# Optimization experiments

Measured on AMD Instinct MI355X. Metric: run time of the kernel, lower is better.

Reference implementation:

```python
import jax, jax.numpy as jnp
import numpy as np

N = 65536   # number of feature vectors (feat_num)
D = 512     # feature dim (feat_size)
NC = 256    # number of unique classes n; N % NC == 0 as required by feat.chunk(n, 0)
EPS = 1e-8  # torch nn.CosineSimilarity eps


def setup_inputs() -> dict:
    key = jax.random.key(0)
    feat = jax.random.normal(key, (N, D), dtype=jnp.float32)
    # contiguous class blocks so chunk(n,0) groups match unique labels (module's implicit assumption)
    label = (jnp.arange(N, dtype=jnp.int32) // (N // NC)).astype(jnp.int32)
    return {"feat": feat, "label": label}


def reference(feat, label):
    n = NC  # len(label.unique()); static by construction
    # per-class centers: mean of each contiguous chunk  -> [n, D]
    centers = feat.reshape(n, N // n, D).mean(axis=1)
    # pairwise cosine similarity (torch CosineSimilarity: dot / (max(|x|,eps)*max(|y|,eps)))
    norms = jnp.sqrt(jnp.sum(centers * centers, axis=1, keepdims=True))  # [n,1]
    normed = centers / jnp.maximum(norms, EPS)
    sim = normed @ normed.T  # [n, n]
    # mask = label1 eq label1^T; labels are unique -> identity mask. Off-diagonal min per row.
    eye = jnp.eye(n, dtype=bool)
    dist_an = jnp.min(jnp.where(eye, jnp.inf, sim), axis=1)  # [n]
    # sum_i (1 - min_j!=i sim[i,j])
    return jnp.sum(1.0 - dist_an)
```

## Files before the change

### kernel.cpp

```cpp
#include <hip/hip_runtime.h>
#include <math.h>

#define NFEAT 65536
#define DIM   512
#define D4    128
#define NCLS  256
#define ROWS_PER_CLASS 256
#define EPSV  1e-8f

typedef float vf4 __attribute__((ext_vector_type(4)));

__global__ __launch_bounds__(1024)
void kA_center_norm(const vf4* __restrict__ feat4, float4* __restrict__ nT4,
                    float* __restrict__ out) {
    const int cls  = blockIdx.x;
    const int t    = threadIdx.x;
    const int col4 = t & 127;
    const int sub  = t >> 7;
    const int row0 = cls * ROWS_PER_CLASS + sub * 32;

    const vf4* p = feat4 + (size_t)row0 * D4 + col4;

    vf4 v[8], w[8];
#pragma unroll
    for (int k = 0; k < 8; ++k)
        v[k] = __builtin_nontemporal_load(p + (size_t)k * D4);

    vf4 acc = (vf4){0.f, 0.f, 0.f, 0.f};
#pragma unroll
    for (int r = 8; r < 32; r += 8) {
#pragma unroll
        for (int k = 0; k < 8; ++k)
            w[k] = __builtin_nontemporal_load(p + (size_t)(r + k) * D4);
#pragma unroll
        for (int k = 0; k < 8; ++k) {
            acc += v[k];
            v[k] = w[k];
        }
    }
#pragma unroll
    for (int k = 0; k < 8; ++k) acc += v[k];

    __shared__ vf4 red[1024];
    red[t] = acc;
    __syncthreads();

    __shared__ float wsum[2];
    __shared__ float s_inv;
    vf4 c = (vf4){0.f, 0.f, 0.f, 0.f};
    if (t < 128) {
        c = red[t];
#pragma unroll
        for (int s = 1; s < 8; ++s) c += red[t + 128 * s];
        const float ms = 1.0f / (float)ROWS_PER_CLASS;
        c *= ms;

        float ss = c.x*c.x + c.y*c.y + c.z*c.z + c.w*c.w;
#pragma unroll
        for (int o = 32; o > 0; o >>= 1) ss += __shfl_down(ss, o, 64);
        if ((t & 63) == 0) wsum[t >> 6] = ss;
    }
    __syncthreads();
    if (t == 0) {
        float nrm = sqrtf(wsum[0] + wsum[1]);
        s_inv = 1.0f / fmaxf(nrm, EPSV);
        if (cls == 0) out[0] = 0.f;
    }
    __syncthreads();
    if (t < 128) {
        c *= s_inv;
        float4 o4 = make_float4(c.x, c.y, c.z, c.w);
        nT4[(size_t)col4 * NCLS + cls] = o4;
    }
}

__global__ __launch_bounds__(1024)
void kB_min_sum(const float4* __restrict__ nT4, float* __restrict__ out) {
    const int j = blockIdx.x;
    const int t = threadIdx.x;

    __shared__ float4 bj[D4];
    __shared__ float  pacc[4][256];
    __shared__ float  wmin[4];
    if (t < D4) bj[t] = nT4[(size_t)t * NCLS + j];
    __syncthreads();

    const int i    = t & 255;
    const int part = t >> 8;
    const int g0   = part * 32;
    float dacc = 0.f;
#pragma unroll 8
    for (int g = g0; g < g0 + 32; ++g) {
        float4 a = nT4[(size_t)g * NCLS + i];
        float4 b = bj[g];
        dacc += a.x*b.x + a.y*b.y + a.z*b.z + a.w*b.w;
    }
    pacc[part][i] = dacc;
    __syncthreads();

    if (t < 256) {
        float d = pacc[0][i] + pacc[1][i] + pacc[2][i] + pacc[3][i];
        if (i == j) d = INFINITY;
#pragma unroll
        for (int o = 32; o > 0; o >>= 1) d = fminf(d, __shfl_down(d, o, 64));
        if ((i & 63) == 0) wmin[i >> 6] = d;
    }
    __syncthreads();
    if (t == 0) {
        float m = fminf(fminf(wmin[0], wmin[1]), fminf(wmin[2], wmin[3]));
        atomicAdd(out, 1.0f - m);
    }
}

extern "C" void kernel_launch(void* const* d_in, const int* in_sizes, int n_in,
                              void* d_out, int out_size, void* d_ws, size_t ws_size,
                              hipStream_t stream) {
    const float* feat = (const float*)d_in[0];
    float* out = (float*)d_out;

    float* nT4f = (float*)d_ws;

    kA_center_norm <<<NCLS, 1024, 0, stream>>>((const vf4*)feat, (float4*)nT4f, out);
    kB_min_sum     <<<NCLS, 1024, 0, stream>>>((const float4*)nT4f, out);
}
```

Measured before the change: 188.2 us.

## Split center reduction into many small partial-sum blocks plus a normalize kernel

The class-center pass is split in two. The first kernel uses 2048 blocks of 128 threads, each summing 32 rows into a partial vector in workspace. A second small kernel combines the 8 partials per class, normalizes, and writes the transposed layout. This spreads the 128 MB streaming read over more, smaller blocks for better occupancy and memory-level parallelism than 256 large blocks, at the cost of an extra launch and a small partial-sum round trip.

```diff
diff --git a/kernel.cpp b/kernel.cpp
--- a/kernel.cpp
+++ b/kernel.cpp
@@ -10,16 +10,13 @@
 
 typedef float vf4 __attribute__((ext_vector_type(4)));
 
-__global__ __launch_bounds__(1024)
-void kA_center_norm(const vf4* __restrict__ feat4, float4* __restrict__ nT4,
-                    float* __restrict__ out) {
-    const int cls  = blockIdx.x;
-    const int t    = threadIdx.x;
-    const int col4 = t & 127;
-    const int sub  = t >> 7;
-    const int row0 = cls * ROWS_PER_CLASS + sub * 32;
+__global__ __launch_bounds__(128, 4)
+void kA1_partial(const vf4* __restrict__ feat4, vf4* __restrict__ part) {
+    const int g = blockIdx.x;
+    const int t = threadIdx.x;
+    const int row0 = (g >> 3) * ROWS_PER_CLASS + (g & 7) * 32;
 
-    const vf4* p = feat4 + (size_t)row0 * D4 + col4;
+    const vf4* p = feat4 + (size_t)row0 * D4 + t;
 
     vf4 v[8], w[8];
 #pragma unroll
@@ -41,37 +38,38 @@
 #pragma unroll
     for (int k = 0; k < 8; ++k) acc += v[k];
 
-    __shared__ vf4 red[1024];
-    red[t] = acc;
-    __syncthreads();
+    part[(size_t)g * 128 + t] = acc;
+}
+
+__global__ __launch_bounds__(128)
+void kA2_norm(const vf4* __restrict__ part, float4* __restrict__ nT4,
+              float* __restrict__ out) {
+    const int c = blockIdx.x;
+    const int t = threadIdx.x;
+
+    const vf4* q = part + (size_t)c * 8 * 128 + t;
+    vf4 cs = q[0];
+#pragma unroll
+    for (int s = 1; s < 8; ++s) cs += q[(size_t)s * 128];
+    const float ms = 1.0f / (float)ROWS_PER_CLASS;
+    cs *= ms;
+
+    float ss = cs.x*cs.x + cs.y*cs.y + cs.z*cs.z + cs.w*cs.w;
+#pragma unroll
+    for (int o = 32; o > 0; o >>= 1) ss += __shfl_down(ss, o, 64);
 
     __shared__ float wsum[2];
     __shared__ float s_inv;
-    vf4 c = (vf4){0.f, 0.f, 0.f, 0.f};
-    if (t < 128) {
-        c = red[t];
-#pragma unroll
-        for (int s = 1; s < 8; ++s) c += red[t + 128 * s];
-        const float ms = 1.0f / (float)ROWS_PER_CLASS;
-        c *= ms;
-
-        float ss = c.x*c.x + c.y*c.y + c.z*c.z + c.w*c.w;
-#pragma unroll
-        for (int o = 32; o > 0; o >>= 1) ss += __shfl_down(ss, o, 64);
-        if ((t & 63) == 0) wsum[t >> 6] = ss;
-    }
+    if ((t & 63) == 0) wsum[t >> 6] = ss;
     __syncthreads();
     if (t == 0) {
         float nrm = sqrtf(wsum[0] + wsum[1]);
         s_inv = 1.0f / fmaxf(nrm, EPSV);
-        if (cls == 0) out[0] = 0.f;
+        if (c == 0) out[0] = 0.f;
     }
     __syncthreads();
-    if (t < 128) {
-        c *= s_inv;
-        float4 o4 = make_float4(c.x, c.y, c.z, c.w);
-        nT4[(size_t)col4 * NCLS + cls] = o4;
-    }
+    cs *= s_inv;
+    nT4[(size_t)t * NCLS + c] = make_float4(cs.x, cs.y, cs.z, cs.w);
 }
 
 __global__ __launch_bounds__(1024)
@@ -85,9 +83,9 @@
     if (t < D4) bj[t] = nT4[(size_t)t * NCLS + j];
     __syncthreads();
 
-    const int i    = t & 255;
-    const int part = t >> 8;
-    const int g0   = part * 32;
+    const int i  = t & 255;
+    const int pt = t >> 8;
+    const int g0 = pt * 32;
     float dacc = 0.f;
 #pragma unroll 8
     for (int g = g0; g < g0 + 32; ++g) {
@@ -95,7 +93,7 @@
         float4 b = bj[g];
         dacc += a.x*b.x + a.y*b.y + a.z*b.z + a.w*b.w;
     }
-    pacc[part][i] = dacc;
+    pacc[pt][i] = dacc;
     __syncthreads();
 
     if (t < 256) {
@@ -119,7 +117,9 @@
     float* out = (float*)d_out;
 
     float* nT4f = (float*)d_ws;
+    vf4*   prt  = (vf4*)((char*)d_ws + 512 * 1024);
 
-    kA_center_norm <<<NCLS, 1024, 0, stream>>>((const vf4*)feat, (float4*)nT4f, out);
-    kB_min_sum     <<<NCLS, 1024, 0, stream>>>((const float4*)nT4f, out);
+    kA1_partial<<<2048, 128, 0, stream>>>((const vf4*)feat, prt);
+    kA2_norm   <<<NCLS,  128, 0, stream>>>(prt, (float4*)nT4f, out);
+    kB_min_sum <<<NCLS, 1024, 0, stream>>>((const float4*)nT4f, out);
 }
```

After: 191.7 us. About the same (+1.9%).

## Stream class rows through double-buffered LDS via global_load_lds in center kernel

Applied to the files above, without the earlier changes.

The per-class reduction kernel now copies feature rows straight from global memory into two 64KB LDS stage buffers with global_load_lds, double-buffering eight 64KB chunks. Each chunk is summed by one group of 128 threads while the next loads. The goal is to keep many loads in flight and skip register staging for this bandwidth-bound 128MB read. In exchange, 128KB of shared memory limits each CU to one block, only one eighth of the threads do adds per chunk, and two barriers per chunk serialize the loop.

```diff
diff --git a/kernel.cpp b/kernel.cpp
--- a/kernel.cpp
+++ b/kernel.cpp
@@ -1,5 +1,6 @@
 #include <hip/hip_runtime.h>
 #include <math.h>
+#include <stdint.h>
 
 #define NFEAT 65536
 #define DIM   512
@@ -10,52 +11,80 @@
 
 typedef float vf4 __attribute__((ext_vector_type(4)));
 
+#define SFENCE() __builtin_amdgcn_sched_barrier(0)
+#define AS1C(p) ((const __attribute__((address_space(1))) void*)(p))
+#define AS3(p)  ((__attribute__((address_space(3))) void*)(p))
+
 __global__ __launch_bounds__(1024)
-void kA_center_norm(const vf4* __restrict__ feat4, float4* __restrict__ nT4,
+void kA_center_norm(const float* __restrict__ feat, float4* __restrict__ nT4,
                     float* __restrict__ out) {
     const int cls  = blockIdx.x;
     const int t    = threadIdx.x;
+    const int w    = t >> 6;
+    const int lane = t & 63;
     const int col4 = t & 127;
     const int sub  = t >> 7;
-    const int row0 = cls * ROWS_PER_CLASS + sub * 32;
 
-    const vf4* p = feat4 + (size_t)row0 * D4 + col4;
+    __shared__ char stage[2][65536];
 
-    vf4 v[8], w[8];
-#pragma unroll
-    for (int k = 0; k < 8; ++k)
-        v[k] = __builtin_nontemporal_load(p + (size_t)k * D4);
+    const char* cbase = (const char*)feat + (size_t)cls * (ROWS_PER_CLASS * DIM * 4);
+    const char* gsrc  = cbase + (size_t)w * 1024 + (size_t)lane * 16;
+
+#define ISSUE(c, p) do {                                                      \
+        const char* g_ = gsrc + (size_t)(c) * 65536;                          \
+        char* l_ = &stage[p][w * 1024];                                       \
+        __builtin_amdgcn_global_load_lds(AS1C(g_),         AS3(l_),         16, 0, 0); \
+        __builtin_amdgcn_global_load_lds(AS1C(g_ + 16384), AS3(l_ + 16384), 16, 0, 0); \
+        __builtin_amdgcn_global_load_lds(AS1C(g_ + 32768), AS3(l_ + 32768), 16, 0, 0); \
+        __builtin_amdgcn_global_load_lds(AS1C(g_ + 49152), AS3(l_ + 49152), 16, 0, 0); \
+    } while (0)
+
+    ISSUE(0, 0);
+    ISSUE(1, 1);
+    SFENCE();
 
     vf4 acc = (vf4){0.f, 0.f, 0.f, 0.f};
+
 #pragma unroll
-    for (int r = 8; r < 32; r += 8) {
-#pragma unroll
-        for (int k = 0; k < 8; ++k)
-            w[k] = __builtin_nontemporal_load(p + (size_t)(r + k) * D4);
-#pragma unroll
-        for (int k = 0; k < 8; ++k) {
-            acc += v[k];
-            v[k] = w[k];
+    for (int c = 0; c < 8; ++c) {
+        if (c < 7) asm volatile("s_waitcnt vmcnt(4)" ::: "memory");
+        else       asm volatile("s_waitcnt vmcnt(0)" ::: "memory");
+        SFENCE();
+        __builtin_amdgcn_s_barrier();
+        SFENCE();
+
+        if (sub == c) {
+            const vf4* src = (const vf4*)&stage[c & 1][0];
+#pragma unroll 8
+            for (int r = 0; r < 32; ++r) acc += src[r * 128 + col4];
         }
+        SFENCE();
+        asm volatile("s_waitcnt lgkmcnt(0)" ::: "memory");
+        SFENCE();
+        __builtin_amdgcn_s_barrier();
+        SFENCE();
+
+        if (c < 6) ISSUE(c + 2, c & 1);
+        SFENCE();
     }
-#pragma unroll
-    for (int k = 0; k < 8; ++k) acc += v[k];
+#undef ISSUE
 
-    __shared__ vf4 red[1024];
+    vf4*   red   = (vf4*)&stage[0][0];
+    float* wsum  = (float*)&stage[1][0];
+    float* s_inv = (float*)&stage[1][8];
+
     red[t] = acc;
     __syncthreads();
 
-    __shared__ float wsum[2];
-    __shared__ float s_inv;
-    vf4 c = (vf4){0.f, 0.f, 0.f, 0.f};
+    vf4 cv = (vf4){0.f, 0.f, 0.f, 0.f};
     if (t < 128) {
-        c = red[t];
+        cv = red[t];
 #pragma unroll
-        for (int s = 1; s < 8; ++s) c += red[t + 128 * s];
+        for (int s = 1; s < 8; ++s) cv += red[t + 128 * s];
         const float ms = 1.0f / (float)ROWS_PER_CLASS;
-        c *= ms;
+        cv *= ms;
 
-        float ss = c.x*c.x + c.y*c.y + c.z*c.z + c.w*c.w;
+        float ss = cv.x*cv.x + cv.y*cv.y + cv.z*cv.z + cv.w*cv.w;
 #pragma unroll
         for (int o = 32; o > 0; o >>= 1) ss += __shfl_down(ss, o, 64);
         if ((t & 63) == 0) wsum[t >> 6] = ss;
@@ -63,14 +92,13 @@
     __syncthreads();
     if (t == 0) {
         float nrm = sqrtf(wsum[0] + wsum[1]);
-        s_inv = 1.0f / fmaxf(nrm, EPSV);
+        *s_inv = 1.0f / fmaxf(nrm, EPSV);
         if (cls == 0) out[0] = 0.f;
     }
     __syncthreads();
     if (t < 128) {
-        c *= s_inv;
-        float4 o4 = make_float4(c.x, c.y, c.z, c.w);
-        nT4[(size_t)col4 * NCLS + cls] = o4;
+        cv *= *s_inv;
+        nT4[(size_t)col4 * NCLS + cls] = make_float4(cv.x, cv.y, cv.z, cv.w);
     }
 }
 
@@ -85,9 +113,9 @@
     if (t < D4) bj[t] = nT4[(size_t)t * NCLS + j];
     __syncthreads();
 
-    const int i    = t & 255;
-    const int part = t >> 8;
-    const int g0   = part * 32;
+    const int i  = t & 255;
+    const int pt = t >> 8;
+    const int g0 = pt * 32;
     float dacc = 0.f;
 #pragma unroll 8
     for (int g = g0; g < g0 + 32; ++g) {
@@ -95,7 +123,7 @@
         float4 b = bj[g];
         dacc += a.x*b.x + a.y*b.y + a.z*b.z + a.w*b.w;
     }
-    pacc[part][i] = dacc;
+    pacc[pt][i] = dacc;
     __syncthreads();
 
     if (t < 256) {
@@ -120,6 +148,6 @@
 
     float* nT4f = (float*)d_ws;
 
-    kA_center_norm <<<NCLS, 1024, 0, stream>>>((const vf4*)feat, (float4*)nT4f, out);
+    kA_center_norm <<<NCLS, 1024, 0, stream>>>(feat, (float4*)nT4f, out);
     kB_min_sum     <<<NCLS, 1024, 0, stream>>>((const float4*)nT4f, out);
 }
```

Measured after the change: 198.8 us. 1.06x slower.
